# Performance work log

Hardware: AMD Instinct MI355X
Metric: run time of the kernel (lower is better)

Reference implementation:

```python
import jax, jax.numpy as jnp
import numpy as np

B, S1, S2, S3 = 2, 64, 64, 40
INIT_STEP, NUM_CH = 10, 1
WIDTH, MODES, TMODES = 64, 12, 8
GRID_DIM = 3
N_LAYERS = 4


def setup_inputs() -> dict:
    key = jax.random.key(0)
    ks = jax.random.split(key, 16)
    scale = 1.0 / (WIDTH * WIDTH)
    d_in = INIT_STEP * NUM_CH + GRID_DIM
    return {
        "x": jax.random.normal(ks[0], (B, S1, S2, S3, INIT_STEP * NUM_CH), jnp.float32),
        "p_w": jax.random.normal(ks[1], (WIDTH, d_in), jnp.float32) * 0.05,
        "p_b": jnp.zeros((WIDTH,), jnp.float32),
        # radial spectral weights (reflection=False): lower-center column + lower-right block, stacked over 4 layers
        "W_LC": scale * jax.random.uniform(ks[2], (N_LAYERS, WIDTH, WIDTH, MODES, 1, TMODES), jnp.float32),
        "W_LR": scale * jax.random.uniform(ks[3], (N_LAYERS, WIDTH, WIDTH, MODES - 1, MODES - 1, TMODES), jnp.float32),
        "mlp_w1": jax.random.normal(ks[4], (N_LAYERS, WIDTH, WIDTH), jnp.float32) * 0.05,
        "mlp_b1": jnp.zeros((N_LAYERS, WIDTH), jnp.float32),
        "mlp_w2": jax.random.normal(ks[5], (N_LAYERS, WIDTH, WIDTH), jnp.float32) * 0.05,
        "mlp_b2": jnp.zeros((N_LAYERS, WIDTH), jnp.float32),
        "w_w": jax.random.normal(ks[6], (N_LAYERS, WIDTH, WIDTH), jnp.float32) * 0.05,
        "w_b": jnp.zeros((N_LAYERS, WIDTH), jnp.float32),
        "q_w1": jax.random.normal(ks[7], (4 * WIDTH, WIDTH), jnp.float32) * 0.05,
        "q_b1": jnp.zeros((4 * WIDTH,), jnp.float32),
        "q_w2": jax.random.normal(ks[8], (NUM_CH, 4 * WIDTH), jnp.float32) * 0.05,
        "q_b2": jnp.zeros((NUM_CH,), jnp.float32),
    }


def _add_grid(x):
    b, s1, s2, s3, _ = x.shape
    gx = jnp.linspace(0.0, 1.0, s1, dtype=x.dtype)
    gy = jnp.linspace(0.0, 1.0, s2, dtype=x.dtype)
    gt = jnp.linspace(0.0, 1.0, s3, dtype=x.dtype)
    g = jnp.stack(jnp.meshgrid(gx, gy, gt, indexing="ij"), axis=-1)  # (s1,s2,s3,3)
    g = jnp.broadcast_to(g[None], (b, s1, s2, s3, GRID_DIM))
    return jnp.concatenate([x, g], axis=-1)


def _rot90(a):
    # torch.rot90(a, k=1, dims=[-3,-2]) == transpose(flip(a, -2), (-3,-2))
    return jnp.swapaxes(jnp.flip(a, axis=-2), -3, -2)


def _spectral_weights(W_LC, W_LR):
    # W_LC: (i,o,m,1,tm), W_LR: (i,o,m-1,m-1,tm) -> full radial weight (i,o,2m-1,2m-1,tm)
    W_LRf = jnp.concatenate([W_LC[:, :, 1:], W_LR], axis=-2)                    # (i,o,m-1,m,tm)
    W_UR = jnp.concatenate([jnp.flip(W_LC, axis=-3), _rot90(W_LRf)], axis=-2)   # (i,o,m,m,tm)
    W_R = jnp.concatenate([W_UR, W_LRf], axis=-3)                               # (i,o,2m-1,m,tm)
    return jnp.concatenate([jnp.flip(W_R[..., 1:, :], axis=(-3, -2)), W_R], axis=-2)


def _spectral_conv(x, W_LC, W_LR):
    b, ci, s1, s2, s3 = x.shape
    f0y, f0x = s1 // 2, s2 // 2  # index of zero freq after fftshift
    W = _spectral_weights(W_LC, W_LR)
    x_ft = jnp.fft.fftshift(jnp.fft.rfftn(x, axes=(-3, -2, -1)), axes=(-3, -2))
    xs = x_ft[..., f0y - MODES + 1:f0y + MODES, f0x - MODES + 1:f0x + MODES, :TMODES]
    out = jnp.einsum("bixyz,ioxyz->boxyz", xs, W.astype(xs.dtype))
    co = W.shape[1]
    out_ft = jnp.zeros((b, co, s1, s2, s3 // 2 + 1), dtype=xs.dtype)
    out_ft = out_ft.at[..., f0y - MODES + 1:f0y + MODES, f0x - MODES + 1:f0x + MODES, :TMODES].set(out)
    return jnp.fft.irfftn(jnp.fft.ifftshift(out_ft, axes=(-3, -2)), s=(s1, s2, s3), axes=(-3, -2, -1))


def _conv1x1(x, w, b):
    return jnp.einsum("bixyz,oi->boxyz", x, w) + b[None, :, None, None, None]


def _mlp3d(x, w1, b1, w2, b2):
    h = jax.nn.gelu(_conv1x1(x, w1, b1), approximate=False)
    return _conv1x1(h, w2, b2)


def _forward(x, p_w, p_b, W_LC, W_LR, mlp_w1, mlp_b1, mlp_w2, mlp_b2, w_w, w_b, q_w1, q_b1, q_w2, q_b2):
    x = _add_grid(x)
    x = jnp.einsum("bxyzi,wi->bxyzw", x, p_w) + p_b
    x = jnp.transpose(x, (0, 4, 1, 2, 3))  # (B, width, S1, S2, S3)
    for l in range(N_LAYERS):
        x1 = _spectral_conv(x, W_LC[l], W_LR[l])
        x1 = _mlp3d(x1, mlp_w1[l], mlp_b1[l], mlp_w2[l], mlp_b2[l])
        x2 = _conv1x1(x, w_w[l], w_b[l])
        x = x1 + x2
        if l < N_LAYERS - 1:
            x = jax.nn.relu(x)
    x = _mlp3d(x, q_w1, q_b1, q_w2, q_b2)
    return jnp.transpose(x, (0, 2, 3, 4, 1))


def reference(x, p_w, p_b, W_LC, W_LR, mlp_w1, mlp_b1, mlp_w2, mlp_b2, w_w, w_b, q_w1, q_b1, q_w2, q_b2):
    return _forward(x, p_w, p_b, W_LC, W_LR, mlp_w1, mlp_b1, mlp_w2, mlp_b2, w_w, w_b, q_w1, q_b1, q_w2, q_b2)
```

## Files before the change

### kernel.cpp

```cpp
#include <hip/hip_runtime.h>
#include <math.h>

#define PI_D 3.14159265358979323846

#define REP64(M) M(0) M(1) M(2) M(3) M(4) M(5) M(6) M(7) M(8) M(9) M(10) M(11) \
    M(12) M(13) M(14) M(15) M(16) M(17) M(18) M(19) M(20) M(21) M(22) M(23) \
    M(24) M(25) M(26) M(27) M(28) M(29) M(30) M(31) M(32) M(33) M(34) M(35) \
    M(36) M(37) M(38) M(39) M(40) M(41) M(42) M(43) M(44) M(45) M(46) M(47) \
    M(48) M(49) M(50) M(51) M(52) M(53) M(54) M(55) M(56) M(57) M(58) M(59) \
    M(60) M(61) M(62) M(63)

__global__ void k_tables(float* tzf, float* tzi, float* tz2, float* txf, float* txi) {
    int t = blockIdx.x * blockDim.x + threadIdx.x;
    if (t < 320) {
        int z = t >> 3, k = t & 7;
        double ang = -2.0 * PI_D * (double)(z * k) / 40.0;
        tzf[t * 2] = (float)cos(ang); tzf[t * 2 + 1] = (float)sin(ang);
        tzi[t * 2] = (float)cos(-ang); tzi[t * 2 + 1] = (float)sin(-ang);
        double s = 1.0 / 163840.0;
        double f = (k == 0) ? s : 2.0 * s;
        tz2[t * 2] = (float)(f * cos(-ang));
        tz2[t * 2 + 1] = (k == 0) ? 0.0f : (float)(-f * sin(-ang));
    }
    if (t < 1472) {
        int xx = t / 23, m = t % 23;
        double ang = -2.0 * PI_D * (double)(xx * (m - 11)) / 64.0;
        txf[t * 2] = (float)cos(ang); txf[t * 2 + 1] = (float)sin(ang);
        txi[t * 2] = (float)cos(-ang); txi[t * 2 + 1] = (float)sin(-ang);
    }
}

__global__ void k_wtrans(const float* __restrict__ w2, const float* __restrict__ ww,
                         const float* __restrict__ w1,
                         float* __restrict__ w2t, float* __restrict__ wwt,
                         float* __restrict__ w1t) {
    int gid = blockIdx.x * blockDim.x + threadIdx.x;
    if (gid < 16384) {
        int l = gid >> 12, r = gid & 4095, o = r >> 6, i = r & 63;
        w2t[l * 4096 + i * 64 + o] = w2[l * 4096 + o * 64 + i];
        wwt[l * 4096 + i * 64 + o] = ww[l * 4096 + o * 64 + i];
        w1t[l * 4096 + i * 64 + o] = w1[l * 4096 + o * 64 + i];
    }
}

__global__ void k_lift(const float* __restrict__ xin, const float* __restrict__ pw,
                       const float* __restrict__ pb, float* __restrict__ xo) {
    int gid = blockIdx.x * 256 + threadIdx.x;
    int b = gid / 163840, p = gid % 163840;
    int y = p / 2560, xx = (p / 40) % 64, z = p % 40;
    float v[13];
#pragma unroll
    for (int i = 0; i < 10; i++) v[i] = xin[(size_t)gid * 10 + i];
    v[10] = (float)((double)y / 63.0);
    v[11] = (float)((double)xx / 63.0);
    v[12] = (float)((double)z / 39.0);
    size_t ob = (size_t)b * 10485760 + p;
    for (int c = 0; c < 64; c++) {
        float a = pb[c];
#pragma unroll
        for (int i = 0; i < 13; i++) a += pw[c * 13 + i] * v[i];
        xo[ob + (size_t)c * 163840] = a;
    }
}

__global__ void k_fwd_zx(const float* __restrict__ x, const float* __restrict__ tzf,
                         const float* __restrict__ txf, float* __restrict__ Fx) {
    int bid = blockIdx.x;
    int b = bid >> 12, c = (bid >> 6) & 63, y = bid & 63;
    int t = threadIdx.x;
    __shared__ float xr_[2560];
    __shared__ float f1[1024];
    __shared__ float tzs[640];
    const float* xrow = x + ((size_t)((b * 64 + c) * 4096 + y * 64)) * 40;
    for (int idx = t; idx < 2560; idx += 256) xr_[idx] = xrow[idx];
    for (int idx = t; idx < 640; idx += 256) tzs[idx] = tzf[idx];
    __syncthreads();
    for (int q = t; q < 512; q += 256) {
        int xx = q >> 3, k = q & 7;
        float sr = 0.f, si = 0.f;
        for (int z = 0; z < 40; z++) {
            float v = xr_[xx * 40 + z];
            sr += v * tzs[(z * 8 + k) * 2];
            si += v * tzs[(z * 8 + k) * 2 + 1];
        }
        f1[(xx * 8 + k) * 2] = sr;
        f1[(xx * 8 + k) * 2 + 1] = si;
    }
    __syncthreads();
    if (t < 184) {
        int m = t >> 3, k = t & 7;
        float sr = 0.f, si = 0.f;
        for (int xx = 0; xx < 64; xx++) {
            float ar = f1[(xx * 8 + k) * 2], ai = f1[(xx * 8 + k) * 2 + 1];
            float tr = txf[(xx * 23 + m) * 2], ti = txf[(xx * 23 + m) * 2 + 1];
            sr += ar * tr - ai * ti;
            si += ar * ti + ai * tr;
        }
        size_t g = ((size_t)(((b * 64 + c) * 64 + y) * 23 + m) * 8 + k) * 2;
        Fx[g] = sr; Fx[g + 1] = si;
    }
}

__global__ void k_fwd_y(const float* __restrict__ Fx, const float* __restrict__ txf,
                        float* __restrict__ Xs) {
    int bid = blockIdx.x;
    int b = bid / 1472, rem = bid % 1472, c = rem / 23, m = rem % 23;
    int t = threadIdx.x;
    __shared__ float s[1024];
    for (int idx = t; idx < 512; idx += 192) {
        int y = idx >> 3, k = idx & 7;
        size_t g = ((size_t)(((b * 64 + c) * 64 + y) * 23 + m) * 8 + k) * 2;
        s[idx * 2] = Fx[g]; s[idx * 2 + 1] = Fx[g + 1];
    }
    __syncthreads();
    if (t < 184) {
        int n = t >> 3, k = t & 7;
        float sr = 0.f, si = 0.f;
        for (int y = 0; y < 64; y++) {
            float ar = s[(y * 8 + k) * 2], ai = s[(y * 8 + k) * 2 + 1];
            float tr = txf[(y * 23 + n) * 2], ti = txf[(y * 23 + n) * 2 + 1];
            sr += ar * tr - ai * ti;
            si += ar * ti + ai * tr;
        }
        size_t g = ((size_t)(((b * 64 + c) * 23 + n) * 23 + m) * 8 + k) * 2;
        Xs[g] = sr; Xs[g + 1] = si;
    }
}

__global__ void k_mix(const float* __restrict__ Xs, const float* __restrict__ WLC,
                      const float* __restrict__ WLR, float* __restrict__ Md) {
    int bid = blockIdx.x;
    int n = bid / 23, m = bid % 23;
    int a = n, c = m, yy, w;
    if (c >= 11) { yy = a; w = c - 11; } else { yy = 22 - a; w = 11 - c; }
    int isLC, idx;
    if (yy >= 12) {
        int p = yy - 12, q = w;
        if (q == 0) { isLC = 1; idx = p + 1; } else { isLC = 0; idx = p * 11 + (q - 1); }
    } else {
        if (w == 0) { isLC = 1; idx = 11 - yy; }
        else {
            int p = w - 1, q = 11 - yy;
            if (q == 0) { isLC = 1; idx = p + 1; } else { isLC = 0; idx = p * 11 + (q - 1); }
        }
    }
    const float* src = isLC ? WLC : WLR;
    int stride = isLC ? 96 : 968;
    int base8 = idx * 8;

    int t = threadIdx.x;
    int o = t >> 3, tt = t & 7;
    __shared__ __align__(16) float wl[8 * 64 * 8];
    __shared__ float xl[256];
    float aR0 = 0.f, aI0 = 0.f, aR1 = 0.f, aI1 = 0.f;
    for (int i0 = 0; i0 < 64; i0 += 8) {
        {
            int il = t >> 6, oo = t & 63;
            const float4* g = (const float4*)(src + (size_t)((i0 + il) * 64 + oo) * stride + base8);
            float4 A = g[0], B = g[1];
            float4* d = (float4*)&wl[(il * 64 + oo) * 8];
            d[0] = A; d[1] = B;
        }
        if (t < 256) {
            int bb = t >> 7, il = (t >> 4) & 7, kk = (t >> 1) & 7, ri = t & 1;
            xl[t] = Xs[((size_t)(((bb * 64 + i0 + il) * 23 + n) * 23 + m) * 8 + kk) * 2 + ri];
        }
        __syncthreads();
#pragma unroll
        for (int il = 0; il < 8; il++) {
            float wv = wl[(il * 64 + o) * 8 + tt];
            float xr0 = xl[(il * 8 + tt) * 2], xi0 = xl[(il * 8 + tt) * 2 + 1];
            float xr1 = xl[128 + (il * 8 + tt) * 2], xi1 = xl[128 + (il * 8 + tt) * 2 + 1];
            aR0 += wv * xr0; aI0 += wv * xi0;
            aR1 += wv * xr1; aI1 += wv * xi1;
        }
        __syncthreads();
    }
    size_t ob0 = ((size_t)((o * 23 + n) * 23 + m) * 8 + tt) * 2;
    size_t ob1 = ((size_t)(((64 + o) * 23 + n) * 23 + m) * 8 + tt) * 2;
    Md[ob0] = aR0; Md[ob0 + 1] = aI0;
    Md[ob1] = aR1; Md[ob1 + 1] = aI1;
}

__global__ void k_inv_y(const float* __restrict__ Md, const float* __restrict__ txi,
                        float* __restrict__ T1) {
    int bid = blockIdx.x;
    int b = bid / 1472, rem = bid % 1472, o = rem / 23, m = rem % 23;
    int t = threadIdx.x;
    __shared__ float s[368];
    if (t < 184) {
        int n = t >> 3, kk = t & 7;
        size_t g = ((size_t)(((b * 64 + o) * 23 + n) * 23 + m) * 8 + kk) * 2;
        s[t * 2] = Md[g]; s[t * 2 + 1] = Md[g + 1];
    }
    __syncthreads();
    int y = t >> 3, k = t & 7;
    float sr = 0.f, si = 0.f;
    for (int n = 0; n < 23; n++) {
        float ar = s[(n * 8 + k) * 2], ai = s[(n * 8 + k) * 2 + 1];
        float tr = txi[(y * 23 + n) * 2], ti = txi[(y * 23 + n) * 2 + 1];
        sr += ar * tr - ai * ti;
        si += ar * ti + ai * tr;
    }
    size_t g = ((size_t)(((b * 64 + o) * 64 + y) * 23 + m) * 8 + k) * 2;
    T1[g] = sr; T1[g + 1] = si;
}

__global__ void k_inv_x(const float* __restrict__ T1, const float* __restrict__ txi,
                        float* __restrict__ T2) {
    int bid = blockIdx.x;
    int b = bid >> 12, o = (bid >> 6) & 63, y = bid & 63;
    int t = threadIdx.x;
    __shared__ float s[368];
    if (t < 184) {
        size_t g = (size_t)(((b * 64 + o) * 64 + y)) * 368 + t * 2;
        s[t * 2] = T1[g]; s[t * 2 + 1] = T1[g + 1];
    }
    __syncthreads();
    int xx = t >> 3, k = t & 7;
    float sr = 0.f, si = 0.f;
    for (int m = 0; m < 23; m++) {
        float ar = s[(m * 8 + k) * 2], ai = s[(m * 8 + k) * 2 + 1];
        float tr = txi[(xx * 23 + m) * 2], ti = txi[(xx * 23 + m) * 2 + 1];
        sr += ar * tr - ai * ti;
        si += ar * ti + ai * tr;
    }
    size_t g = ((size_t)((b * 64 + o) * 4096 + y * 64 + xx) * 8 + k) * 2;
    T2[g] = sr; T2[g + 1] = si;
}

__device__ __forceinline__ float gelu_fast(float x) {
    float u = x * 0.70710678118654752f;
    float a = fabsf(u);
    float t = 1.0f / (1.0f + 0.3275911f * a);
    float poly = t * (0.254829592f + t * (-0.284496736f + t * (1.421413741f +
                 t * (-1.453152027f + t * 1.061405429f))));
    float erfa = 1.0f - poly * __expf(-a * a);
    float er = copysignf(erfa, u);
    return 0.5f * x * (1.0f + er);
}

__global__ __launch_bounds__(256) void k_mlp1(
    const float* __restrict__ t2buf, const float* __restrict__ w1t,
    const float* __restrict__ b1, const float* __restrict__ tz2g,
    float* __restrict__ g) {
    __shared__ __align__(16) float T2s[4096];
    __shared__ __align__(16) float w1ls[4096];
    __shared__ __align__(16) float Hs[4096];
    __shared__ float tzls[640];
    int t = threadIdx.x;
    int site0 = blockIdx.x * 4;
    for (int idx = t; idx < 1024; idx += 256) {
        int sl = idx >> 8, r = idx & 255, i = r >> 2, q = r & 3;
        int site = site0 + sl;
        int b = site >> 12, yx = site & 4095;
        const float4* src = (const float4*)(t2buf + ((size_t)(b * 64 + i) * 4096 + yx) * 16 + q * 4);
        *(float4*)&T2s[sl * 1024 + i * 16 + q * 4] = *src;
    }
    for (int idx = t; idx < 1024; idx += 256)
        *(float4*)&w1ls[idx * 4] = ((const float4*)w1t)[idx];
    for (int idx = t; idx < 640; idx += 256) tzls[idx] = tz2g[idx];
    __syncthreads();
    {
        int sl = t >> 6, u = t & 63;
        int j0 = (u >> 2) * 4, kr0 = (u & 3) * 4;
        float c0 = 0.f, c1 = 0.f, c2 = 0.f, c3 = 0.f, c4 = 0.f, c5 = 0.f, c6 = 0.f, c7 = 0.f;
        float c8 = 0.f, c9 = 0.f, c10 = 0.f, c11 = 0.f, c12 = 0.f, c13 = 0.f, c14 = 0.f, c15 = 0.f;
        int tb = sl * 1024 + kr0;
        for (int i = 0; i < 64; i++) {
            float4 W = *(const float4*)&w1ls[i * 64 + j0];
            float4 T = *(const float4*)&T2s[tb + i * 16];
            c0  = fmaf(W.x, T.x, c0);  c1  = fmaf(W.x, T.y, c1);
            c2  = fmaf(W.x, T.z, c2);  c3  = fmaf(W.x, T.w, c3);
            c4  = fmaf(W.y, T.x, c4);  c5  = fmaf(W.y, T.y, c5);
            c6  = fmaf(W.y, T.z, c6);  c7  = fmaf(W.y, T.w, c7);
            c8  = fmaf(W.z, T.x, c8);  c9  = fmaf(W.z, T.y, c9);
            c10 = fmaf(W.z, T.z, c10); c11 = fmaf(W.z, T.w, c11);
            c12 = fmaf(W.w, T.x, c12); c13 = fmaf(W.w, T.y, c13);
            c14 = fmaf(W.w, T.z, c14); c15 = fmaf(W.w, T.w, c15);
        }
        int hb = sl * 1024 + j0 * 16 + kr0;
        *(float4*)&Hs[hb]      = make_float4(c0, c1, c2, c3);
        *(float4*)&Hs[hb + 16] = make_float4(c4, c5, c6, c7);
        *(float4*)&Hs[hb + 32] = make_float4(c8, c9, c10, c11);
        *(float4*)&Hs[hb + 48] = make_float4(c12, c13, c14, c15);
    }
    __syncthreads();
    {
        int sl = t >> 6, j = t & 63;
        int site = site0 + sl;
        int b = site >> 12, yx = site & 4095;
        int hb = sl * 1024 + j * 16;
        float4 H0 = *(const float4*)&Hs[hb];
        float4 H1 = *(const float4*)&Hs[hb + 4];
        float4 H2 = *(const float4*)&Hs[hb + 8];
        float4 H3 = *(const float4*)&Hs[hb + 12];
        float b1j = b1[j];
        size_t obase = (size_t)j * 327680 + (size_t)b * 163840 + yx * 40;
        for (int zc = 0; zc < 10; zc++) {
            float4 outv;
#pragma unroll
            for (int zi = 0; zi < 4; zi++) {
                int z = zc * 4 + zi;
                const float4* tz = (const float4*)&tzls[z * 16];
                float4 T0 = tz[0], T1v = tz[1], T2v = tz[2], T3 = tz[3];
                float v = H0.x * T0.x;
                v = fmaf(H0.y, T0.y, v); v = fmaf(H0.z, T0.z, v); v = fmaf(H0.w, T0.w, v);
                v = fmaf(H1.x, T1v.x, v); v = fmaf(H1.y, T1v.y, v);
                v = fmaf(H1.z, T1v.z, v); v = fmaf(H1.w, T1v.w, v);
                v = fmaf(H2.x, T2v.x, v); v = fmaf(H2.y, T2v.y, v);
                v = fmaf(H2.z, T2v.z, v); v = fmaf(H2.w, T2v.w, v);
                v = fmaf(H3.x, T3.x, v); v = fmaf(H3.y, T3.y, v);
                v = fmaf(H3.z, T3.z, v); v = fmaf(H3.w, T3.w, v);
                float h = b1j + v;
                float gv = gelu_fast(h);
                if (zi == 0) outv.x = gv; else if (zi == 1) outv.y = gv;
                else if (zi == 2) outv.z = gv; else outv.w = gv;
            }
            *(float4*)&g[obase + zc * 4] = outv;
        }
    }
}

#define FMA8x4(W0, W1, X) \
    a0  = fmaf(W0.x, X.x, a0);  a1  = fmaf(W0.x, X.y, a1);  a2  = fmaf(W0.x, X.z, a2);  a3  = fmaf(W0.x, X.w, a3); \
    a4  = fmaf(W0.y, X.x, a4);  a5  = fmaf(W0.y, X.y, a5);  a6  = fmaf(W0.y, X.z, a6);  a7  = fmaf(W0.y, X.w, a7); \
    a8  = fmaf(W0.z, X.x, a8);  a9  = fmaf(W0.z, X.y, a9);  a10 = fmaf(W0.z, X.z, a10); a11 = fmaf(W0.z, X.w, a11); \
    a12 = fmaf(W0.w, X.x, a12); a13 = fmaf(W0.w, X.y, a13); a14 = fmaf(W0.w, X.z, a14); a15 = fmaf(W0.w, X.w, a15); \
    a16 = fmaf(W1.x, X.x, a16); a17 = fmaf(W1.x, X.y, a17); a18 = fmaf(W1.x, X.z, a18); a19 = fmaf(W1.x, X.w, a19); \
    a20 = fmaf(W1.y, X.x, a20); a21 = fmaf(W1.y, X.y, a21); a22 = fmaf(W1.y, X.z, a22); a23 = fmaf(W1.y, X.w, a23); \
    a24 = fmaf(W1.z, X.x, a24); a25 = fmaf(W1.z, X.y, a25); a26 = fmaf(W1.z, X.z, a26); a27 = fmaf(W1.z, X.w, a27); \
    a28 = fmaf(W1.w, X.x, a28); a29 = fmaf(W1.w, X.y, a29); a30 = fmaf(W1.w, X.z, a30); a31 = fmaf(W1.w, X.w, a31);

__global__ __launch_bounds__(256) void k_mlp2(
    const float* __restrict__ g, float* __restrict__ x,
    const float* __restrict__ w2t, const float* __restrict__ b2,
    const float* __restrict__ wwt, const float* __restrict__ wb, int dorelu) {
    __shared__ __align__(16) float vs[8192];
    __shared__ __align__(16) float wls[4096];
    int t = threadIdx.x;
    int P0 = blockIdx.x * 128;
    int b = P0 / 163840, pl = P0 % 163840;
    size_t xbase = (size_t)b * 10485760 + pl;
    for (int idx = t; idx < 2048; idx += 256) {
        int i = idx >> 5, pp = (idx & 31) * 4;
        *(float4*)&vs[i * 128 + pp] = *(const float4*)(x + xbase + (size_t)i * 163840 + pp);
    }
    for (int idx = t; idx < 1024; idx += 256)
        *(float4*)&wls[idx * 4] = ((const float4*)wwt)[idx];
    int o0 = (t >> 5) * 8, p0 = (t & 31) * 4;
    float a0  = b2[o0]     + wb[o0],     a1  = a0, a2  = a0, a3  = a0;
    float a4  = b2[o0 + 1] + wb[o0 + 1], a5  = a4, a6  = a4, a7  = a4;
    float a8  = b2[o0 + 2] + wb[o0 + 2], a9  = a8, a10 = a8, a11 = a8;
    float a12 = b2[o0 + 3] + wb[o0 + 3], a13 = a12, a14 = a12, a15 = a12;
    float a16 = b2[o0 + 4] + wb[o0 + 4], a17 = a16, a18 = a16, a19 = a16;
    float a20 = b2[o0 + 5] + wb[o0 + 5], a21 = a20, a22 = a20, a23 = a20;
    float a24 = b2[o0 + 6] + wb[o0 + 6], a25 = a24, a26 = a24, a27 = a24;
    float a28 = b2[o0 + 7] + wb[o0 + 7], a29 = a28, a30 = a28, a31 = a28;
    __syncthreads();
    for (int i = 0; i < 64; i++) {
        const float4* wp = (const float4*)&wls[i * 64 + o0];
        float4 W0 = wp[0], W1 = wp[1];
        float4 X = *(const float4*)&vs[i * 128 + p0];
        FMA8x4(W0, W1, X)
    }
    __syncthreads();
    for (int idx = t; idx < 2048; idx += 256) {
        int j = idx >> 5, pp = (idx & 31) * 4;
        *(float4*)&vs[j * 128 + pp] = *(const float4*)(g + (size_t)j * 327680 + P0 + pp);
    }
    for (int idx = t; idx < 1024; idx += 256)
        *(float4*)&wls[idx * 4] = ((const float4*)w2t)[idx];
    __syncthreads();
    for (int j = 0; j < 64; j++) {
        const float4* wp = (const float4*)&wls[j * 64 + o0];
        float4 W0 = wp[0], W1 = wp[1];
        float4 X = *(const float4*)&vs[j * 128 + p0];
        FMA8x4(W0, W1, X)
    }
#define STROW(oo, r0, r1, r2, r3) { \
        float4 R; \
        if (dorelu) R = make_float4(fmaxf(r0, 0.f), fmaxf(r1, 0.f), fmaxf(r2, 0.f), fmaxf(r3, 0.f)); \
        else R = make_float4(r0, r1, r2, r3); \
        *(float4*)(x + xbase + (size_t)(o0 + oo) * 163840 + p0) = R; }
    STROW(0, a0, a1, a2, a3)
    STROW(1, a4, a5, a6, a7)
    STROW(2, a8, a9, a10, a11)
    STROW(3, a12, a13, a14, a15)
    STROW(4, a16, a17, a18, a19)
    STROW(5, a20, a21, a22, a23)
    STROW(6, a24, a25, a26, a27)
    STROW(7, a28, a29, a30, a31)
#undef STROW
}

#define FR24(V, PA, PB, n0, n1, n2, n3) \
    PA = fmaf(V.x, xa##n0, PA); PB = fmaf(V.x, xb##n0, PB); \
    PA = fmaf(V.y, xa##n1, PA); PB = fmaf(V.y, xb##n1, PB); \
    PA = fmaf(V.z, xa##n2, PA); PB = fmaf(V.z, xb##n2, PB); \
    PA = fmaf(V.w, xa##n3, PA); PB = fmaf(V.w, xb##n3, PB);

#define FMAROW2_ALL(wb) { const float4* _w = (wb); float4 V; \
    V=_w[0];  FR24(V,pa0,pb0,0,1,2,3)     V=_w[1];  FR24(V,pa1,pb1,4,5,6,7) \
    V=_w[2];  FR24(V,pa2,pb2,8,9,10,11)   V=_w[3];  FR24(V,pa3,pb3,12,13,14,15) \
    V=_w[4];  FR24(V,pa0,pb0,16,17,18,19) V=_w[5];  FR24(V,pa1,pb1,20,21,22,23) \
    V=_w[6];  FR24(V,pa2,pb2,24,25,26,27) V=_w[7];  FR24(V,pa3,pb3,28,29,30,31) \
    V=_w[8];  FR24(V,pa0,pb0,32,33,34,35) V=_w[9];  FR24(V,pa1,pb1,36,37,38,39) \
    V=_w[10]; FR24(V,pa2,pb2,40,41,42,43) V=_w[11]; FR24(V,pa3,pb3,44,45,46,47) \
    V=_w[12]; FR24(V,pa0,pb0,48,49,50,51) V=_w[13]; FR24(V,pa1,pb1,52,53,54,55) \
    V=_w[14]; FR24(V,pa2,pb2,56,57,58,59) V=_w[15]; FR24(V,pa3,pb3,60,61,62,63) }

__global__ __launch_bounds__(256, 3) void k_head(
    const float* __restrict__ xcur,
    const float* __restrict__ qw1, const float* __restrict__ qb1,
    const float* __restrict__ qw2, const float* __restrict__ qb2,
    float* __restrict__ outp) {
    __shared__ float4 wls[1024];
    int t = threadIdx.x;
    int P0 = blockIdx.x * 512;
    int b = P0 / 163840, pl = P0 % 163840;
    size_t baseA = (size_t)b * 10485760 + pl + t;
    size_t baseB = baseA + 256;
#define LDA(n) float xa##n = xcur[baseA + (size_t)(n) * 163840];
    REP64(LDA)
#undef LDA
#define LDB(n) float xb##n = xcur[baseB + (size_t)(n) * 163840];
    REP64(LDB)
#undef LDB
    float accA = qb2[0], accB = qb2[0];
    for (int c = 0; c < 4; c++) {
        __syncthreads();
        const float4* src = (const float4*)(qw1 + c * 4096);
        for (int idx = t; idx < 1024; idx += 256) wls[idx] = src[idx];
        __syncthreads();
        for (int jl = 0; jl < 64; jl++) {
            int j = c * 64 + jl;
            float pa0 = 0.f, pa1 = 0.f, pa2 = 0.f, pa3 = 0.f;
            float pb0 = 0.f, pb1 = 0.f, pb2 = 0.f, pb3 = 0.f;
            FMAROW2_ALL(&wls[jl * 16])
            float bj = qb1[j], wj = qw2[j];
            float hA = bj + ((pa0 + pa1) + (pa2 + pa3));
            float hB = bj + ((pb0 + pb1) + (pb2 + pb3));
            accA += wj * gelu_fast(hA);
            accB += wj * gelu_fast(hB);
        }
    }
    outp[P0 + t] = accA;
    outp[P0 + 256 + t] = accB;
}

extern "C" void kernel_launch(void* const* d_in, const int* in_sizes, int n_in,
                              void* d_out, int out_size, void* d_ws, size_t ws_size,
                              hipStream_t stream) {
    const float* x_in = (const float*)d_in[0];
    const float* p_w  = (const float*)d_in[1];
    const float* p_b  = (const float*)d_in[2];
    const float* W_LC = (const float*)d_in[3];
    const float* W_LR = (const float*)d_in[4];
    const float* m_w1 = (const float*)d_in[5];
    const float* m_b1 = (const float*)d_in[6];
    const float* m_w2 = (const float*)d_in[7];
    const float* m_b2 = (const float*)d_in[8];
    const float* w_w  = (const float*)d_in[9];
    const float* w_b  = (const float*)d_in[10];
    const float* q_w1 = (const float*)d_in[11];
    const float* q_b1 = (const float*)d_in[12];
    const float* q_w2 = (const float*)d_in[13];
    const float* q_b2 = (const float*)d_in[14];

    char* ws = (char*)d_ws;
    float* tzf = (float*)(ws + 0);
    float* tzi = (float*)(ws + 2560);
    float* tz2 = (float*)(ws + 5120);
    float* txf = (float*)(ws + 7680);
    float* txi = (float*)(ws + 19456);
    float* w2t = (float*)(ws + 32768);
    float* wwt = (float*)(ws + 98304);
    float* w1t = (float*)(ws + 163840);
    size_t off = 229376;
    float* xA = (float*)(ws + off); off += 83886080ull;
    float* gbuf = (float*)(ws + off); off += 83886080ull;
    float* Fx = (float*)(ws + off); off += 12058624ull;
    float* Xs = (float*)(ws + off); off += 4333568ull;
    float* Md = (float*)(ws + off); off += 4333568ull;
    float* T1 = (float*)(ws + off); off += 12058624ull;
    float* T2 = (float*)(ws + off); off += 33554432ull;

    k_tables<<<6, 256, 0, stream>>>(tzf, tzi, tz2, txf, txi);
    k_wtrans<<<64, 256, 0, stream>>>(m_w2, w_w, m_w1, w2t, wwt, w1t);
    k_lift<<<1280, 256, 0, stream>>>(x_in, p_w, p_b, xA);

    for (int l = 0; l < 4; l++) {
        k_fwd_zx<<<8192, 256, 0, stream>>>(xA, tzf, txf, Fx);
        k_fwd_y<<<2944, 192, 0, stream>>>(Fx, txf, Xs);
        k_mix<<<529, 512, 0, stream>>>(Xs, W_LC + (size_t)l * 393216,
                                       W_LR + (size_t)l * 3964928, Md);
        k_inv_y<<<2944, 512, 0, stream>>>(Md, txi, T1);
        k_inv_x<<<8192, 512, 0, stream>>>(T1, txi, T2);
        k_mlp1<<<2048, 256, 0, stream>>>(T2, w1t + (size_t)l * 4096, m_b1 + l * 64,
                                         tz2, gbuf);
        k_mlp2<<<2560, 256, 0, stream>>>(gbuf, xA, w2t + (size_t)l * 4096, m_b2 + l * 64,
                                         wwt + (size_t)l * 4096, w_b + l * 64,
                                         (l < 3) ? 1 : 0);
    }
    k_head<<<640, 256, 0, stream>>>(xA, q_w1, q_b1, q_w2, q_b2, (float*)d_out);
}
```

Before: 1.563 ms.

## Vectorize DFT stage kernels, cache twiddles in LDS, restructure mlp2 tiling

The forward and inverse DFT stage kernels now stage the x-twiddle tables in shared memory, add a k-major z-twiddle table, use float2/float4 loads and stores, and compute two outputs per thread with smaller blocks. k_mlp2 drops its shared activation tile, reads activations straight from global memory, and has each thread handle 8 channels by 8 points, halving the grid. The aim is fewer scalar global and shared accesses and more register reuse. In exchange, each block reloads the twiddle tables and mlp2 carries more registers per thread.

```diff
diff --git a/kernel.cpp b/kernel.cpp
--- a/kernel.cpp
+++ b/kernel.cpp
@@ -10,7 +10,8 @@
     M(48) M(49) M(50) M(51) M(52) M(53) M(54) M(55) M(56) M(57) M(58) M(59) \
     M(60) M(61) M(62) M(63)
 
-__global__ void k_tables(float* tzf, float* tzi, float* tz2, float* txf, float* txi) {
+__global__ void k_tables(float* tzf, float* tzi, float* tz2, float* tzk,
+                         float* txf, float* txi) {
     int t = blockIdx.x * blockDim.x + threadIdx.x;
     if (t < 320) {
         int z = t >> 3, k = t & 7;
@@ -21,6 +22,8 @@
         double f = (k == 0) ? s : 2.0 * s;
         tz2[t * 2] = (float)(f * cos(-ang));
         tz2[t * 2 + 1] = (k == 0) ? 0.0f : (float)(-f * sin(-ang));
+        tzk[(k * 40 + z) * 2] = (float)cos(ang);
+        tzk[(k * 40 + z) * 2 + 1] = (float)sin(ang);
     }
     if (t < 1472) {
         int xx = t / 23, m = t % 23;
@@ -63,67 +66,91 @@
     }
 }
 
-__global__ void k_fwd_zx(const float* __restrict__ x, const float* __restrict__ tzf,
-                         const float* __restrict__ txf, float* __restrict__ Fx) {
+__global__ __launch_bounds__(256) void k_fwd_zx(const float* __restrict__ x,
+        const float* __restrict__ tzk, const float* __restrict__ txf,
+        float* __restrict__ Fx) {
     int bid = blockIdx.x;
     int b = bid >> 12, c = (bid >> 6) & 63, y = bid & 63;
     int t = threadIdx.x;
-    __shared__ float xr_[2560];
-    __shared__ float f1[1024];
-    __shared__ float tzs[640];
-    const float* xrow = x + ((size_t)((b * 64 + c) * 4096 + y * 64)) * 40;
-    for (int idx = t; idx < 2560; idx += 256) xr_[idx] = xrow[idx];
-    for (int idx = t; idx < 640; idx += 256) tzs[idx] = tzf[idx];
-    __syncthreads();
-    for (int q = t; q < 512; q += 256) {
-        int xx = q >> 3, k = q & 7;
-        float sr = 0.f, si = 0.f;
-        for (int z = 0; z < 40; z++) {
-            float v = xr_[xx * 40 + z];
-            sr += v * tzs[(z * 8 + k) * 2];
-            si += v * tzs[(z * 8 + k) * 2 + 1];
-        }
-        f1[(xx * 8 + k) * 2] = sr;
-        f1[(xx * 8 + k) * 2 + 1] = si;
+    __shared__ __align__(16) float xr_[2560];
+    __shared__ __align__(16) float tzs[672];
+    __shared__ __align__(16) float txs[2944];
+    __shared__ __align__(16) float f1[1024];
+    const float4* xrow4 = (const float4*)(x + ((size_t)((b * 64 + c) * 4096 + y * 64)) * 40);
+    for (int idx = t; idx < 640; idx += 256) ((float4*)xr_)[idx] = xrow4[idx];
+    for (int idx = t; idx < 160; idx += 256) {
+        int k = idx / 20, q = idx % 20;
+        ((float4*)tzs)[k * 21 + q] = ((const float4*)tzk)[idx];
+    }
+    for (int idx = t; idx < 736; idx += 256) ((float4*)txs)[idx] = ((const float4*)txf)[idx];
+    __syncthreads();
+    {
+        int xx = t >> 3, k = t & 7;
+        float sr0 = 0.f, si0 = 0.f, sr1 = 0.f, si1 = 0.f;
+        const float2* tzp = (const float2*)(tzs + k * 84);
+        const float4* X0 = (const float4*)(xr_ + xx * 40);
+        const float4* X1 = (const float4*)(xr_ + (xx + 32) * 40);
+        for (int zc = 0; zc < 10; zc++) {
+            float4 A = X0[zc], B = X1[zc];
+            float2 T0 = tzp[zc * 4], T1v = tzp[zc * 4 + 1];
+            float2 T2v = tzp[zc * 4 + 2], T3v = tzp[zc * 4 + 3];
+            sr0 = fmaf(A.x, T0.x, sr0);  si0 = fmaf(A.x, T0.y, si0);
+            sr0 = fmaf(A.y, T1v.x, sr0); si0 = fmaf(A.y, T1v.y, si0);
+            sr0 = fmaf(A.z, T2v.x, sr0); si0 = fmaf(A.z, T2v.y, si0);
+            sr0 = fmaf(A.w, T3v.x, sr0); si0 = fmaf(A.w, T3v.y, si0);
+            sr1 = fmaf(B.x, T0.x, sr1);  si1 = fmaf(B.x, T0.y, si1);
+            sr1 = fmaf(B.y, T1v.x, sr1); si1 = fmaf(B.y, T1v.y, si1);
+            sr1 = fmaf(B.z, T2v.x, sr1); si1 = fmaf(B.z, T2v.y, si1);
+            sr1 = fmaf(B.w, T3v.x, sr1); si1 = fmaf(B.w, T3v.y, si1);
+        }
+        ((float2*)f1)[xx * 8 + k] = make_float2(sr0, si0);
+        ((float2*)f1)[(xx + 32) * 8 + k] = make_float2(sr1, si1);
     }
     __syncthreads();
     if (t < 184) {
         int m = t >> 3, k = t & 7;
         float sr = 0.f, si = 0.f;
+        const float2* f1p = (const float2*)f1;
+        const float2* txp = (const float2*)txs;
         for (int xx = 0; xx < 64; xx++) {
-            float ar = f1[(xx * 8 + k) * 2], ai = f1[(xx * 8 + k) * 2 + 1];
-            float tr = txf[(xx * 23 + m) * 2], ti = txf[(xx * 23 + m) * 2 + 1];
-            sr += ar * tr - ai * ti;
-            si += ar * ti + ai * tr;
+            float2 a = f1p[xx * 8 + k];
+            float2 w = txp[xx * 23 + m];
+            sr = fmaf(a.x, w.x, sr); sr = fmaf(-a.y, w.y, sr);
+            si = fmaf(a.x, w.y, si); si = fmaf(a.y, w.x, si);
         }
         size_t g = ((size_t)(((b * 64 + c) * 64 + y) * 23 + m) * 8 + k) * 2;
         Fx[g] = sr; Fx[g + 1] = si;
     }
 }
 
-__global__ void k_fwd_y(const float* __restrict__ Fx, const float* __restrict__ txf,
-                        float* __restrict__ Xs) {
+__global__ __launch_bounds__(128) void k_fwd_y(const float* __restrict__ Fx,
+        const float* __restrict__ txf, float* __restrict__ Xs) {
     int bid = blockIdx.x;
     int b = bid / 1472, rem = bid % 1472, c = rem / 23, m = rem % 23;
     int t = threadIdx.x;
-    __shared__ float s[1024];
-    for (int idx = t; idx < 512; idx += 192) {
+    __shared__ __align__(16) float s[1024];
+    __shared__ __align__(16) float txs[2944];
+    for (int idx = t; idx < 512; idx += 128) {
         int y = idx >> 3, k = idx & 7;
-        size_t g = ((size_t)(((b * 64 + c) * 64 + y) * 23 + m) * 8 + k) * 2;
-        s[idx * 2] = Fx[g]; s[idx * 2 + 1] = Fx[g + 1];
-    }
-    __syncthreads();
-    if (t < 184) {
-        int n = t >> 3, k = t & 7;
-        float sr = 0.f, si = 0.f;
+        size_t g = ((size_t)(((b * 64 + c) * 64 + y) * 23 + m) * 8 + k);
+        ((float2*)s)[idx] = ((const float2*)Fx)[g];
+    }
+    for (int idx = t; idx < 736; idx += 128) ((float4*)txs)[idx] = ((const float4*)txf)[idx];
+    __syncthreads();
+    if (t < 92) {
+        int n = t >> 2, kp = t & 3;
+        float sr0 = 0.f, si0 = 0.f, sr1 = 0.f, si1 = 0.f;
+        const float2* txp = (const float2*)txs;
         for (int y = 0; y < 64; y++) {
-            float ar = s[(y * 8 + k) * 2], ai = s[(y * 8 + k) * 2 + 1];
-            float tr = txf[(y * 23 + n) * 2], ti = txf[(y * 23 + n) * 2 + 1];
-            sr += ar * tr - ai * ti;
-            si += ar * ti + ai * tr;
-        }
-        size_t g = ((size_t)(((b * 64 + c) * 23 + n) * 23 + m) * 8 + k) * 2;
-        Xs[g] = sr; Xs[g + 1] = si;
+            float4 S = *(const float4*)&s[y * 16 + kp * 4];
+            float2 w = txp[y * 23 + n];
+            sr0 = fmaf(S.x, w.x, sr0); sr0 = fmaf(-S.y, w.y, sr0);
+            si0 = fmaf(S.x, w.y, si0); si0 = fmaf(S.y, w.x, si0);
+            sr1 = fmaf(S.z, w.x, sr1); sr1 = fmaf(-S.w, w.y, sr1);
+            si1 = fmaf(S.z, w.y, si1); si1 = fmaf(S.w, w.x, si1);
+        }
+        size_t g = ((size_t)(((b * 64 + c) * 23 + n) * 23 + m)) * 16 + kp * 4;
+        *(float4*)&Xs[g] = make_float4(sr0, si0, sr1, si1);
     }
 }
 
@@ -182,51 +209,61 @@
     Md[ob1] = aR1; Md[ob1 + 1] = aI1;
 }
 
-__global__ void k_inv_y(const float* __restrict__ Md, const float* __restrict__ txi,
-                        float* __restrict__ T1) {
+__global__ __launch_bounds__(256) void k_inv_y(const float* __restrict__ Md,
+        const float* __restrict__ txi, float* __restrict__ T1) {
     int bid = blockIdx.x;
     int b = bid / 1472, rem = bid % 1472, o = rem / 23, m = rem % 23;
     int t = threadIdx.x;
-    __shared__ float s[368];
+    __shared__ __align__(16) float s[368];
+    __shared__ __align__(16) float txs[2944];
     if (t < 184) {
         int n = t >> 3, kk = t & 7;
-        size_t g = ((size_t)(((b * 64 + o) * 23 + n) * 23 + m) * 8 + kk) * 2;
-        s[t * 2] = Md[g]; s[t * 2 + 1] = Md[g + 1];
-    }
-    __syncthreads();
-    int y = t >> 3, k = t & 7;
-    float sr = 0.f, si = 0.f;
+        size_t g = ((size_t)(((b * 64 + o) * 23 + n) * 23 + m) * 8 + kk);
+        ((float2*)s)[t] = ((const float2*)Md)[g];
+    }
+    for (int idx = t; idx < 736; idx += 256) ((float4*)txs)[idx] = ((const float4*)txi)[idx];
+    __syncthreads();
+    int y = t >> 2, kp = t & 3;
+    float sr0 = 0.f, si0 = 0.f, sr1 = 0.f, si1 = 0.f;
+    const float2* txp = (const float2*)txs;
     for (int n = 0; n < 23; n++) {
-        float ar = s[(n * 8 + k) * 2], ai = s[(n * 8 + k) * 2 + 1];
-        float tr = txi[(y * 23 + n) * 2], ti = txi[(y * 23 + n) * 2 + 1];
-        sr += ar * tr - ai * ti;
-        si += ar * ti + ai * tr;
-    }
-    size_t g = ((size_t)(((b * 64 + o) * 64 + y) * 23 + m) * 8 + k) * 2;
-    T1[g] = sr; T1[g + 1] = si;
-}
-
-__global__ void k_inv_x(const float* __restrict__ T1, const float* __restrict__ txi,
-                        float* __restrict__ T2) {
+        float4 S = *(const float4*)&s[n * 16 + kp * 4];
+        float2 w = txp[y * 23 + n];
+        sr0 = fmaf(S.x, w.x, sr0); sr0 = fmaf(-S.y, w.y, sr0);
+        si0 = fmaf(S.x, w.y, si0); si0 = fmaf(S.y, w.x, si0);
+        sr1 = fmaf(S.z, w.x, sr1); sr1 = fmaf(-S.w, w.y, sr1);
+        si1 = fmaf(S.z, w.y, si1); si1 = fmaf(S.w, w.x, si1);
+    }
+    size_t g = ((size_t)(((b * 64 + o) * 64 + y) * 23 + m)) * 16 + kp * 4;
+    *(float4*)&T1[g] = make_float4(sr0, si0, sr1, si1);
+}
+
+__global__ __launch_bounds__(256) void k_inv_x(const float* __restrict__ T1,
+        const float* __restrict__ txi, float* __restrict__ T2) {
     int bid = blockIdx.x;
     int b = bid >> 12, o = (bid >> 6) & 63, y = bid & 63;
     int t = threadIdx.x;
-    __shared__ float s[368];
-    if (t < 184) {
-        size_t g = (size_t)(((b * 64 + o) * 64 + y)) * 368 + t * 2;
-        s[t * 2] = T1[g]; s[t * 2 + 1] = T1[g + 1];
-    }
-    __syncthreads();
-    int xx = t >> 3, k = t & 7;
-    float sr = 0.f, si = 0.f;
+    __shared__ __align__(16) float s[368];
+    __shared__ __align__(16) float txs[2944];
+    {
+        const float4* src = (const float4*)(T1 + (size_t)((b * 64 + o) * 64 + y) * 368);
+        if (t < 92) ((float4*)s)[t] = src[t];
+    }
+    for (int idx = t; idx < 736; idx += 256) ((float4*)txs)[idx] = ((const float4*)txi)[idx];
+    __syncthreads();
+    int xx = t >> 2, kp = t & 3;
+    float sr0 = 0.f, si0 = 0.f, sr1 = 0.f, si1 = 0.f;
+    const float2* txp = (const float2*)txs;
     for (int m = 0; m < 23; m++) {
-        float ar = s[(m * 8 + k) * 2], ai = s[(m * 8 + k) * 2 + 1];
-        float tr = txi[(xx * 23 + m) * 2], ti = txi[(xx * 23 + m) * 2 + 1];
-        sr += ar * tr - ai * ti;
-        si += ar * ti + ai * tr;
-    }
-    size_t g = ((size_t)((b * 64 + o) * 4096 + y * 64 + xx) * 8 + k) * 2;
-    T2[g] = sr; T2[g + 1] = si;
+        float4 S = *(const float4*)&s[m * 16 + kp * 4];
+        float2 w = txp[xx * 23 + m];
+        sr0 = fmaf(S.x, w.x, sr0); sr0 = fmaf(-S.y, w.y, sr0);
+        si0 = fmaf(S.x, w.y, si0); si0 = fmaf(S.y, w.x, si0);
+        sr1 = fmaf(S.z, w.x, sr1); sr1 = fmaf(-S.w, w.y, sr1);
+        si1 = fmaf(S.z, w.y, si1); si1 = fmaf(S.w, w.x, si1);
+    }
+    size_t g = ((size_t)((b * 64 + o) * 4096 + y * 64 + xx)) * 16 + kp * 4;
+    *(float4*)&T2[g] = make_float4(sr0, si0, sr1, si1);
 }
 
 __device__ __forceinline__ float gelu_fast(float x) {
@@ -322,75 +359,62 @@
     }
 }
 
-#define FMA8x4(W0, W1, X) \
-    a0  = fmaf(W0.x, X.x, a0);  a1  = fmaf(W0.x, X.y, a1);  a2  = fmaf(W0.x, X.z, a2);  a3  = fmaf(W0.x, X.w, a3); \
-    a4  = fmaf(W0.y, X.x, a4);  a5  = fmaf(W0.y, X.y, a5);  a6  = fmaf(W0.y, X.z, a6);  a7  = fmaf(W0.y, X.w, a7); \
-    a8  = fmaf(W0.z, X.x, a8);  a9  = fmaf(W0.z, X.y, a9);  a10 = fmaf(W0.z, X.z, a10); a11 = fmaf(W0.z, X.w, a11); \
-    a12 = fmaf(W0.w, X.x, a12); a13 = fmaf(W0.w, X.y, a13); a14 = fmaf(W0.w, X.z, a14); a15 = fmaf(W0.w, X.w, a15); \
-    a16 = fmaf(W1.x, X.x, a16); a17 = fmaf(W1.x, X.y, a17); a18 = fmaf(W1.x, X.z, a18); a19 = fmaf(W1.x, X.w, a19); \
-    a20 = fmaf(W1.y, X.x, a20); a21 = fmaf(W1.y, X.y, a21); a22 = fmaf(W1.y, X.z, a22); a23 = fmaf(W1.y, X.w, a23); \
-    a24 = fmaf(W1.z, X.x, a24); a25 = fmaf(W1.z, X.y, a25); a26 = fmaf(W1.z, X.z, a26); a27 = fmaf(W1.z, X.w, a27); \
-    a28 = fmaf(W1.w, X.x, a28); a29 = fmaf(W1.w, X.y, a29); a30 = fmaf(W1.w, X.z, a30); a31 = fmaf(W1.w, X.w, a31);
+#define FMAR8(R, Wc) \
+    a##R##0 = fmaf(Wc, X0.x, a##R##0); a##R##1 = fmaf(Wc, X0.y, a##R##1); \
+    a##R##2 = fmaf(Wc, X0.z, a##R##2); a##R##3 = fmaf(Wc, X0.w, a##R##3); \
+    a##R##4 = fmaf(Wc, X1.x, a##R##4); a##R##5 = fmaf(Wc, X1.y, a##R##5); \
+    a##R##6 = fmaf(Wc, X1.z, a##R##6); a##R##7 = fmaf(Wc, X1.w, a##R##7);
 
 __global__ __launch_bounds__(256) void k_mlp2(
     const float* __restrict__ g, float* __restrict__ x,
     const float* __restrict__ w2t, const float* __restrict__ b2,
     const float* __restrict__ wwt, const float* __restrict__ wb, int dorelu) {
-    __shared__ __align__(16) float vs[8192];
     __shared__ __align__(16) float wls[4096];
     int t = threadIdx.x;
-    int P0 = blockIdx.x * 128;
+    int P0 = blockIdx.x * 256;
     int b = P0 / 163840, pl = P0 % 163840;
     size_t xbase = (size_t)b * 10485760 + pl;
-    for (int idx = t; idx < 2048; idx += 256) {
-        int i = idx >> 5, pp = (idx & 31) * 4;
-        *(float4*)&vs[i * 128 + pp] = *(const float4*)(x + xbase + (size_t)i * 163840 + pp);
-    }
+    int o0 = (t >> 5) * 8, p0 = (t & 31) * 8;
+#define INITR(R) float a##R##0 = b2[o0 + R] + wb[o0 + R]; \
+    float a##R##1 = a##R##0, a##R##2 = a##R##0, a##R##3 = a##R##0, \
+          a##R##4 = a##R##0, a##R##5 = a##R##0, a##R##6 = a##R##0, a##R##7 = a##R##0;
+    INITR(0) INITR(1) INITR(2) INITR(3) INITR(4) INITR(5) INITR(6) INITR(7)
+#undef INITR
     for (int idx = t; idx < 1024; idx += 256)
-        *(float4*)&wls[idx * 4] = ((const float4*)wwt)[idx];
-    int o0 = (t >> 5) * 8, p0 = (t & 31) * 4;
-    float a0  = b2[o0]     + wb[o0],     a1  = a0, a2  = a0, a3  = a0;
-    float a4  = b2[o0 + 1] + wb[o0 + 1], a5  = a4, a6  = a4, a7  = a4;
-    float a8  = b2[o0 + 2] + wb[o0 + 2], a9  = a8, a10 = a8, a11 = a8;
-    float a12 = b2[o0 + 3] + wb[o0 + 3], a13 = a12, a14 = a12, a15 = a12;
-    float a16 = b2[o0 + 4] + wb[o0 + 4], a17 = a16, a18 = a16, a19 = a16;
-    float a20 = b2[o0 + 5] + wb[o0 + 5], a21 = a20, a22 = a20, a23 = a20;
-    float a24 = b2[o0 + 6] + wb[o0 + 6], a25 = a24, a26 = a24, a27 = a24;
-    float a28 = b2[o0 + 7] + wb[o0 + 7], a29 = a28, a30 = a28, a31 = a28;
+        ((float4*)wls)[idx] = ((const float4*)wwt)[idx];
     __syncthreads();
     for (int i = 0; i < 64; i++) {
         const float4* wp = (const float4*)&wls[i * 64 + o0];
         float4 W0 = wp[0], W1 = wp[1];
-        float4 X = *(const float4*)&vs[i * 128 + p0];
-        FMA8x4(W0, W1, X)
-    }
-    __syncthreads();
-    for (int idx = t; idx < 2048; idx += 256) {
-        int j = idx >> 5, pp = (idx & 31) * 4;
-        *(float4*)&vs[j * 128 + pp] = *(const float4*)(g + (size_t)j * 327680 + P0 + pp);
-    }
+        const float* xp = x + xbase + (size_t)i * 163840 + p0;
+        float4 X0 = *(const float4*)xp, X1 = *(const float4*)(xp + 4);
+        FMAR8(0, W0.x) FMAR8(1, W0.y) FMAR8(2, W0.z) FMAR8(3, W0.w)
+        FMAR8(4, W1.x) FMAR8(5, W1.y) FMAR8(6, W1.z) FMAR8(7, W1.w)
+    }
+    __syncthreads();
     for (int idx = t; idx < 1024; idx += 256)
-        *(float4*)&wls[idx * 4] = ((const float4*)w2t)[idx];
+        ((float4*)wls)[idx] = ((const float4*)w2t)[idx];
     __syncthreads();
     for (int j = 0; j < 64; j++) {
         const float4* wp = (const float4*)&wls[j * 64 + o0];
         float4 W0 = wp[0], W1 = wp[1];
-        float4 X = *(const float4*)&vs[j * 128 + p0];
-        FMA8x4(W0, W1, X)
-    }
-#define STROW(oo, r0, r1, r2, r3) { \
-        float4 R; \
-        if (dorelu) R = make_float4(fmaxf(r0, 0.f), fmaxf(r1, 0.f), fmaxf(r2, 0.f), fmaxf(r3, 0.f)); \
-        else R = make_float4(r0, r1, r2, r3); \
-        *(float4*)(x + xbase + (size_t)(o0 + oo) * 163840 + p0) = R; }
-    STROW(0, a0, a1, a2, a3)
-    STROW(1, a4, a5, a6, a7)
-    STROW(2, a8, a9, a10, a11)
-    STROW(3, a12, a13, a14, a15)
-    STROW(4, a16, a17, a18, a19)
-    STROW(5, a20, a21, a22, a23)
-    STROW(6, a24, a25, a26, a27)
-    STROW(7, a28, a29, a30, a31)
+        const float* gp = g + (size_t)j * 327680 + P0 + p0;
+        float4 X0 = *(const float4*)gp, X1 = *(const float4*)(gp + 4);
+        FMAR8(0, W0.x) FMAR8(1, W0.y) FMAR8(2, W0.z) FMAR8(3, W0.w)
+        FMAR8(4, W1.x) FMAR8(5, W1.y) FMAR8(6, W1.z) FMAR8(7, W1.w)
+    }
+#define STROW(R) { \
+        float4 R0, R1; \
+        if (dorelu) { \
+            R0 = make_float4(fmaxf(a##R##0, 0.f), fmaxf(a##R##1, 0.f), fmaxf(a##R##2, 0.f), fmaxf(a##R##3, 0.f)); \
+            R1 = make_float4(fmaxf(a##R##4, 0.f), fmaxf(a##R##5, 0.f), fmaxf(a##R##6, 0.f), fmaxf(a##R##7, 0.f)); \
+        } else { \
+            R0 = make_float4(a##R##0, a##R##1, a##R##2, a##R##3); \
+            R1 = make_float4(a##R##4, a##R##5, a##R##6, a##R##7); \
+        } \
+        float* op = x + xbase + (size_t)(o0 + R) * 163840 + p0; \
+        *(float4*)op = R0; *(float4*)(op + 4) = R1; }
+    STROW(0) STROW(1) STROW(2) STROW(3) STROW(4) STROW(5) STROW(6) STROW(7)
 #undef STROW
 }
 
@@ -472,12 +496,13 @@
     float* tzf = (float*)(ws + 0);
     float* tzi = (float*)(ws + 2560);
     float* tz2 = (float*)(ws + 5120);
-    float* txf = (float*)(ws + 7680);
-    float* txi = (float*)(ws + 19456);
-    float* w2t = (float*)(ws + 32768);
-    float* wwt = (float*)(ws + 98304);
-    float* w1t = (float*)(ws + 163840);
-    size_t off = 229376;
+    float* tzk = (float*)(ws + 7680);
+    float* txf = (float*)(ws + 10240);
+    float* txi = (float*)(ws + 22016);
+    float* w2t = (float*)(ws + 65536);
+    float* wwt = (float*)(ws + 131072);
+    float* w1t = (float*)(ws + 196608);
+    size_t off = 262144;
     float* xA = (float*)(ws + off); off += 83886080ull;
     float* gbuf = (float*)(ws + off); off += 83886080ull;
     float* Fx = (float*)(ws + off); off += 12058624ull;
@@ -486,20 +511,20 @@
     float* T1 = (float*)(ws + off); off += 12058624ull;
     float* T2 = (float*)(ws + off); off += 33554432ull;
 
-    k_tables<<<6, 256, 0, stream>>>(tzf, tzi, tz2, txf, txi);
+    k_tables<<<6, 256, 0, stream>>>(tzf, tzi, tz2, tzk, txf, txi);
     k_wtrans<<<64, 256, 0, stream>>>(m_w2, w_w, m_w1, w2t, wwt, w1t);
     k_lift<<<1280, 256, 0, stream>>>(x_in, p_w, p_b, xA);
 
     for (int l = 0; l < 4; l++) {
-        k_fwd_zx<<<8192, 256, 0, stream>>>(xA, tzf, txf, Fx);
-        k_fwd_y<<<2944, 192, 0, stream>>>(Fx, txf, Xs);
+        k_fwd_zx<<<8192, 256, 0, stream>>>(xA, tzk, txf, Fx);
+        k_fwd_y<<<2944, 128, 0, stream>>>(Fx, txf, Xs);
         k_mix<<<529, 512, 0, stream>>>(Xs, W_LC + (size_t)l * 393216,
                                        W_LR + (size_t)l * 3964928, Md);
-        k_inv_y<<<2944, 512, 0, stream>>>(Md, txi, T1);
-        k_inv_x<<<8192, 512, 0, stream>>>(T1, txi, T2);
+        k_inv_y<<<2944, 256, 0, stream>>>(Md, txi, T1);
+        k_inv_x<<<8192, 256, 0, stream>>>(T1, txi, T2);
         k_mlp1<<<2048, 256, 0, stream>>>(T2, w1t + (size_t)l * 4096, m_b1 + l * 64,
                                          tz2, gbuf);
-        k_mlp2<<<2560, 256, 0, stream>>>(gbuf, xA, w2t + (size_t)l * 4096, m_b2 + l * 64,
+        k_mlp2<<<1280, 256, 0, stream>>>(gbuf, xA, w2t + (size_t)l * 4096, m_b2 + l * 64,
                                          wwt + (size_t)l * 4096, w_b + l * 64,
                                          (l < 3) ? 1 : 0);
     }
```

Result: faster. 1.300 ms (-16.8%).
